# Performance work log

Hardware: AMD Instinct MI355X
Metric: run time of the kernel (lower is better)

Reference implementation:

```python
import jax, jax.numpy as jnp
import numpy as np

CLS_NUM, INPUT_DIM, BATCH = 1024, 512, 16384
TAU = 0.1       # gumbel-softmax temperature from F.gumbel_softmax(sim, tau=0.1)
EPS = 1e-12     # F.normalize eps


def _l2norm(x):
    # F.normalize(x, p=2, dim=1)
    n = jnp.sqrt(jnp.sum(x * x, axis=1, keepdims=True))
    return x / jnp.maximum(n, EPS)


def setup_inputs() -> dict:
    key = jax.random.key(0)
    k1, k2, k3 = jax.random.split(key, 3)
    # xavier_uniform bound for [cls_num, input_dim]
    bound = float(np.sqrt(6.0 / (CLS_NUM + INPUT_DIM)))
    return {
        "input": jax.random.normal(k1, (BATCH, INPUT_DIM), dtype=jnp.float32),
        "prototypes_para": jax.random.uniform(k2, (CLS_NUM, INPUT_DIM), dtype=jnp.float32, minval=-bound, maxval=bound),
        "gumbel_u": jax.random.uniform(k3, (BATCH, CLS_NUM), dtype=jnp.float32, minval=1e-6, maxval=1.0 - 1e-6),
    }


def reference(input, prototypes_para, gumbel_u):
    x = _l2norm(input)                 # [B, D]
    p = _l2norm(prototypes_para)       # [K, D]
    # Original: broadcast x and p to [B, K, D] (via multiply-by-ones) then cosine.
    # Since both are unit-norm, cosine similarity == dot product -> one matmul.
    # Input is .detach()'d in the original, so stop_gradient on x here.
    sim = jax.lax.stop_gradient(x) @ p.T                    # [B, K]
    # Gumbel-softmax (soft): softmax((logits + gumbel)/tau)
    g = -jnp.log(-jnp.log(gumbel_u))
    e = jax.nn.softmax((sim + g) / TAU, axis=-1)            # [B, K]
    pt = jnp.einsum('bk,kv->bv', e, p)                      # [B, D]
    sim_loss = jnp.mean(1.0 - jnp.einsum('bk,bk->b', e, sim))
    # Nested i!=j pairwise cosine loop == sum of P P^T minus its diagonal
    ppt = p @ p.T                                           # [K, K]
    div_loss = jnp.sum(ppt) - jnp.sum(jnp.diagonal(ppt))
    return pt, p, sim_loss, div_loss
```

## Files before the change

### kernel.cpp

```cpp
#include <hip/hip_runtime.h>
#include <math.h>

#define B  16384
#define K  1024
#define D  512
#define TAU_INV 10.0f
#define EPS 1e-12f

#define SM_C1 14.426950408889634f
#define SM_C2 5.287663729448977f

typedef unsigned short ushort_t;

#define LOG2F(x) __builtin_amdgcn_logf(x)
#define EXP2F(x) __builtin_amdgcn_exp2f(x)

#define OUT_PT   0
#define OUT_P    (B*D)
#define OUT_SIM  (B*D + K*D)
#define OUT_DIV  (B*D + K*D + 1)

#define WS_RED   1024
#define WS_SIM   32768
#define WS_PH    (WS_SIM + (B*K)/2)
#define WS_PTH   (WS_PH + (K*D)/2)
#define WS_DIAGP (WS_PTH + (K*D)/2)
#define WS_COLP  (WS_DIAGP + 256)


typedef _Float16 half8 __attribute__((ext_vector_type(8)));
typedef float f32x4 __attribute__((ext_vector_type(4)));

__device__ __forceinline__ float wave_reduce_sum(float v) {
    #pragma unroll
    for (int off = 32; off >= 1; off >>= 1) v += __shfl_down(v, off);
    return v;
}
__device__ __forceinline__ float wave_reduce_max(float v) {
    #pragma unroll
    for (int off = 32; off >= 1; off >>= 1) v = fmaxf(v, __shfl_down(v, off));
    return v;
}

__device__ __forceinline__ ushort_t f2h(float f) {
    _Float16 h = (_Float16)f;
    return __builtin_bit_cast(ushort_t, h);
}
__device__ __forceinline__ float h2f(ushort_t u) {
    return (float)__builtin_bit_cast(_Float16, u);
}

__device__ __forceinline__ void async16(const void* g, void* l) {
    __builtin_amdgcn_global_load_lds(
        (const __attribute__((address_space(1))) unsigned int*)g,
        (__attribute__((address_space(3))) unsigned int*)l, 16, 0, 0);
}

__global__ __launch_bounds__(256) void norm_p_kernel(const float* __restrict__ proto,
                                                     float* __restrict__ out,
                                                     float* __restrict__ ws,
                                                     ushort_t* __restrict__ Ph) {
    __shared__ float cs[4][512];
    __shared__ float red[4];
    int tid = threadIdx.x, wid = tid >> 6, lane = tid & 63;
    int row = blockIdx.x * 4 + wid;
    const float4* pr = (const float4*)(proto + (size_t)row * D);
    float4 a = pr[lane * 2], b = pr[lane * 2 + 1];
    float ss = a.x*a.x + a.y*a.y + a.z*a.z + a.w*a.w
             + b.x*b.x + b.y*b.y + b.z*b.z + b.w*b.w;
    ss = wave_reduce_sum(ss);
    ss = __shfl(ss, 0);
    float inv = 1.0f / fmaxf(sqrtf(ss), EPS);
    float4 na = make_float4(a.x*inv, a.y*inv, a.z*inv, a.w*inv);
    float4 nb = make_float4(b.x*inv, b.y*inv, b.z*inv, b.w*inv);
    float4* po = (float4*)(out + OUT_P + (size_t)row * D);
    po[lane * 2]     = na;
    po[lane * 2 + 1] = nb;
    ushort4* ph = (ushort4*)(Ph + (size_t)row * D);
    ph[lane * 2]     = make_ushort4(f2h(na.x), f2h(na.y), f2h(na.z), f2h(na.w));
    ph[lane * 2 + 1] = make_ushort4(f2h(nb.x), f2h(nb.y), f2h(nb.z), f2h(nb.w));
    *(float4*)(&cs[wid][lane * 8])     = na;
    *(float4*)(&cs[wid][lane * 8 + 4]) = nb;
    if (lane == 0) red[wid] = ss * inv * inv;
    __syncthreads();
    float c0 = cs[0][tid] + cs[1][tid] + cs[2][tid] + cs[3][tid];
    float c1 = cs[0][tid + 256] + cs[1][tid + 256] + cs[2][tid + 256] + cs[3][tid + 256];
    ws[WS_COLP + (size_t)blockIdx.x * 512 + tid]       = c0;
    ws[WS_COLP + (size_t)blockIdx.x * 512 + tid + 256] = c1;
    if (tid == 0) ws[WS_DIAGP + blockIdx.x] = red[0] + red[1] + red[2] + red[3];
}

__global__ __launch_bounds__(256) void ptcvt_kernel(const float* __restrict__ out,
                                                    ushort_t* __restrict__ PT) {
    __shared__ float tile[64][65];
    int k0 = blockIdx.x * 64, d0 = blockIdx.y * 64;
    int tid = threadIdx.x;
    const float* phat = out + OUT_P;
    #pragma unroll
    for (int i = tid; i < 64 * 64; i += 256) {
        int kk = i >> 6, dd = i & 63;
        tile[dd][kk] = phat[(size_t)(k0 + kk) * D + d0 + dd];
    }
    __syncthreads();
    #pragma unroll
    for (int i = tid; i < 64 * 64; i += 256) {
        int dd = i >> 6, kk = i & 63;
        PT[(size_t)(d0 + dd) * K + k0 + kk] = f2h(tile[dd][kk]);
    }
}

__global__ __launch_bounds__(256) void xcvt_kernel(const float* __restrict__ x,
                                                   ushort_t* __restrict__ Xh) {
    int wid = threadIdx.x >> 6, lane = threadIdx.x & 63;
    int row = blockIdx.x * 4 + wid;
    const float4* xr = (const float4*)(x + (size_t)row * D);
    float4 a = xr[lane * 2], b = xr[lane * 2 + 1];
    float ss = a.x*a.x + a.y*a.y + a.z*a.z + a.w*a.w
             + b.x*b.x + b.y*b.y + b.z*b.z + b.w*b.w;
    ss = wave_reduce_sum(ss);
    ss = __shfl(ss, 0);
    float inv = 1.0f / fmaxf(sqrtf(ss), EPS);
    ushort4 h0 = make_ushort4(f2h(a.x*inv), f2h(a.y*inv), f2h(a.z*inv), f2h(a.w*inv));
    ushort4 h1 = make_ushort4(f2h(b.x*inv), f2h(b.y*inv), f2h(b.z*inv), f2h(b.w*inv));
    ushort4* xo = (ushort4*)(Xh + (size_t)row * D);
    xo[lane * 2]     = h0;
    xo[lane * 2 + 1] = h1;
}

template<int LDA, int LDB, int LDC, int KK, bool F16C>
__global__ __launch_bounds__(256) void gemm_bt2(const ushort_t* __restrict__ A,
                                                const ushort_t* __restrict__ Bm,
                                                void* __restrict__ Cv) {
    __shared__ __align__(16) ushort_t As[2 * 128 * 32];
    __shared__ __align__(16) ushort_t Bs[2 * 128 * 32];
    int tid = threadIdx.x;
    int wid = tid >> 6, lane = tid & 63;
    int quad = lane >> 4, l16 = lane & 15;
    int wm = (wid & 1) * 64, wn = (wid >> 1) * 64;
    int bn0 = blockIdx.x * 128, bm0 = blockIdx.y * 128;
    int ldrow = lane >> 2;
    int lcol  = (lane & 3) * 8;

    f32x4 acc[4][4] = {};

    ushort_t* AsD[2][2] = {
        { As + (wid * 16) * 32,        As + (64 + wid * 16) * 32 },
        { As + 4096 + (wid * 16) * 32, As + 4096 + (64 + wid * 16) * 32 } };
    ushort_t* BsD[2][2] = {
        { Bs + (wid * 16) * 32,        Bs + (64 + wid * 16) * 32 },
        { Bs + 4096 + (wid * 16) * 32, Bs + 4096 + (64 + wid * 16) * 32 } };

    const ushort_t* Ab = A + (size_t)(bm0 + wid * 16 + ldrow) * LDA + lcol;
    const ushort_t* Bb = Bm + (size_t)(bn0 + wid * 16 + ldrow) * LDB + lcol;

    for (int kc = 0; kc < KK; kc += 64) {
        async16(Ab + kc,                       AsD[0][0]);
        async16(Ab + kc + (size_t)64 * LDA,    AsD[0][1]);
        async16(Ab + kc + 32,                  AsD[1][0]);
        async16(Ab + kc + 32 + (size_t)64*LDA, AsD[1][1]);
        async16(Bb + kc,                       BsD[0][0]);
        async16(Bb + kc + (size_t)64 * LDB,    BsD[0][1]);
        async16(Bb + kc + 32,                  BsD[1][0]);
        async16(Bb + kc + 32 + (size_t)64*LDB, BsD[1][1]);
        __syncthreads();
        #pragma unroll
        for (int p = 0; p < 2; ++p) {
            half8 af[4], bg[4];
            #pragma unroll
            for (int i = 0; i < 4; ++i)
                af[i] = *(const half8*)(As + p * 4096 + (wm + 16 * i + l16) * 32 + quad * 8);
            #pragma unroll
            for (int j = 0; j < 4; ++j)
                bg[j] = *(const half8*)(Bs + p * 4096 + (wn + 16 * j + l16) * 32 + quad * 8);
            #pragma unroll
            for (int i = 0; i < 4; ++i)
                #pragma unroll
                for (int j = 0; j < 4; ++j)
                    acc[i][j] = __builtin_amdgcn_mfma_f32_16x16x32_f16(af[i], bg[j], acc[i][j], 0, 0, 0);
        }
        __syncthreads();
    }
    #pragma unroll
    for (int i = 0; i < 4; ++i) {
        #pragma unroll
        for (int j = 0; j < 4; ++j) {
            #pragma unroll
            for (int r = 0; r < 4; ++r) {
                int row = bm0 + wm + 16 * i + quad * 4 + r;
                int col = bn0 + wn + 16 * j + l16;
                if (F16C)
                    ((ushort_t*)Cv)[(size_t)row * LDC + col] = f2h(acc[i][j][r]);
                else
                    ((float*)Cv)[(size_t)row * LDC + col] = acc[i][j][r];
            }
        }
    }
}

__global__ __launch_bounds__(256) void softmax_rows(const float* __restrict__ u,
                                                    float* __restrict__ ws) {
    ushort_t* simh = (ushort_t*)(ws + WS_SIM);
    int tid = threadIdx.x;
    int wid = tid >> 6, lane = tid & 63;
    int gw = blockIdx.x * 4 + wid;
    float dotacc = 0.0f;

    for (int r = 0; r < 4; ++r) {
        int row = gw + 4096 * r;
        ushort4* srow = (ushort4*)(simh + (size_t)row * K);
        const float4* urow = (const float4*)(u + (size_t)row * K);
        float4 s[4], z[4];
        #pragma unroll
        for (int j = 0; j < 4; ++j) {
            ushort4 sh = srow[lane + 64 * j];
            float4 uu = urow[lane + 64 * j];
            s[j] = make_float4(h2f(sh.x), h2f(sh.y), h2f(sh.z), h2f(sh.w));
            z[j].x = SM_C1 * s[j].x - 10.0f * LOG2F(-LOG2F(uu.x)) + SM_C2;
            z[j].y = SM_C1 * s[j].y - 10.0f * LOG2F(-LOG2F(uu.y)) + SM_C2;
            z[j].z = SM_C1 * s[j].z - 10.0f * LOG2F(-LOG2F(uu.z)) + SM_C2;
            z[j].w = SM_C1 * s[j].w - 10.0f * LOG2F(-LOG2F(uu.w)) + SM_C2;
        }
        float m = z[0].x;
        #pragma unroll
        for (int j = 0; j < 4; ++j)
            m = fmaxf(m, fmaxf(fmaxf(z[j].x, z[j].y), fmaxf(z[j].z, z[j].w)));
        m = wave_reduce_max(m);
        m = __shfl(m, 0);

        float4 e[4];
        float l = 0.0f;
        #pragma unroll
        for (int j = 0; j < 4; ++j) {
            e[j].x = EXP2F(z[j].x - m);
            e[j].y = EXP2F(z[j].y - m);
            e[j].z = EXP2F(z[j].z - m);
            e[j].w = EXP2F(z[j].w - m);
            l += e[j].x + e[j].y + e[j].z + e[j].w;
        }
        l = wave_reduce_sum(l);
        l = __shfl(l, 0);
        float inv = 1.0f / l;

        #pragma unroll
        for (int j = 0; j < 4; ++j) {
            float ex = e[j].x * inv, ey = e[j].y * inv,
                  ez = e[j].z * inv, ew = e[j].w * inv;
            srow[lane + 64 * j] = make_ushort4(f2h(ex), f2h(ey), f2h(ez), f2h(ew));
            dotacc += ex * s[j].x + ey * s[j].y + ez * s[j].z + ew * s[j].w;
        }
    }

    dotacc = wave_reduce_sum(dotacc);
    __shared__ float red[4];
    if (lane == 0) red[wid] = dotacc;
    __syncthreads();
    if (tid == 0) ws[WS_RED + blockIdx.x] = red[0] + red[1] + red[2] + red[3];
}

__global__ __launch_bounds__(1024) void finalize_kernel(float* __restrict__ out,
                                                        const float* __restrict__ ws) {
    __shared__ float cred[1024];
    __shared__ float rd[16], rs[16], rg[16];
    int tid = threadIdx.x, wid = tid >> 6, lane = tid & 63;
    int col = tid & 511, h = tid >> 9;
    float c = 0.0f;
    #pragma unroll 8
    for (int b2 = h * 128; b2 < h * 128 + 128; ++b2)
        c += ws[WS_COLP + (size_t)b2 * 512 + col];
    cred[tid] = c;
    float vdot = ws[WS_RED + tid];
    float diag = (tid < 256) ? ws[WS_DIAGP + tid] : 0.0f;
    __syncthreads();
    float vssq = 0.0f;
    if (tid < 512) {
        float cc = cred[tid] + cred[tid + 512];
        vssq = cc * cc;
    }
    vdot = wave_reduce_sum(vdot);
    vssq = wave_reduce_sum(vssq);
    diag = wave_reduce_sum(diag);
    if (lane == 0) { rd[wid] = vdot; rs[wid] = vssq; rg[wid] = diag; }
    __syncthreads();
    if (tid == 0) {
        float dot = 0.0f, ssq = 0.0f, dg = 0.0f;
        #pragma unroll
        for (int w = 0; w < 16; ++w) { dot += rd[w]; ssq += rs[w]; dg += rg[w]; }
        out[OUT_SIM] = 1.0f - dot * (1.0f / (float)B);
        out[OUT_DIV] = ssq - dg;
    }
}

extern "C" void kernel_launch(void* const* d_in, const int* in_sizes, int n_in,
                              void* d_out, int out_size, void* d_ws, size_t ws_size,
                              hipStream_t stream) {
    const float* input  = (const float*)d_in[0];
    const float* proto  = (const float*)d_in[1];
    const float* gumbel = (const float*)d_in[2];
    float* out = (float*)d_out;
    float* ws  = (float*)d_ws;

    ushort_t* Xh   = (ushort_t*)(out + OUT_PT);
    ushort_t* Ph   = (ushort_t*)(ws + WS_PH);
    ushort_t* PTh  = (ushort_t*)(ws + WS_PTH);
    ushort_t* simh = (ushort_t*)(ws + WS_SIM);

    norm_p_kernel<<<K / 4, 256, 0, stream>>>(proto, out, ws, Ph);
    {
        dim3 grid(K / 64, D / 64);
        ptcvt_kernel<<<grid, 256, 0, stream>>>(out, PTh);
    }
    xcvt_kernel<<<B / 4, 256, 0, stream>>>(input, Xh);
    {
        dim3 grid(K / 128, B / 128);
        gemm_bt2<512, 512, K, 512, true><<<grid, 256, 0, stream>>>(Xh, Ph, simh);
    }
    softmax_rows<<<1024, 256, 0, stream>>>(gumbel, ws);
    {
        dim3 grid(D / 128, B / 128);
        gemm_bt2<1024, 1024, D, 1024, false><<<grid, 256, 0, stream>>>(simh, PTh, out + OUT_PT);
    }
    finalize_kernel<<<1, 1024, 0, stream>>>(out, ws);
}
```

Measured before the change: 216.1 us.

## Replace 128x128 GEMM with 256-row double-buffered swizzled-LDS GEMM

Replaces the 128x128-tile GEMM with a templated 512-thread kernel using 256xBN tiles and 64-wide K slices. Shared-memory staging is now double-buffered and XOR-swizzled, with prefetch of the next slice interleaved into four compute phases and ordered by vmcnt waits and barriers. The larger tiles raise operand reuse per global load, the prefetch overlaps loads with MFMA work, and the swizzle avoids LDS bank conflicts. In exchange the kernel uses more registers and shared memory per block, and the grid shrinks, which may hurt occupancy or wave balance across CUs.

```diff
diff --git a/kernel.cpp b/kernel.cpp
--- a/kernel.cpp
+++ b/kernel.cpp
@@ -4,7 +4,6 @@
 #define B  16384
 #define K  1024
 #define D  512
-#define TAU_INV 10.0f
 #define EPS 1e-12f
 
 #define SM_C1 14.426950408889634f
@@ -127,63 +126,110 @@
     xo[lane * 2 + 1] = h1;
 }
 
-template<int LDA, int LDB, int LDC, int KK, bool F16C>
-__global__ __launch_bounds__(256) void gemm_bt2(const ushort_t* __restrict__ A,
-                                                const ushort_t* __restrict__ Bm,
-                                                void* __restrict__ Cv) {
-    __shared__ __align__(16) ushort_t As[2 * 128 * 32];
-    __shared__ __align__(16) ushort_t Bs[2 * 128 * 32];
+template<int BN, int LDA, int LDB, int LDC, int KK, bool F16C>
+__global__ __launch_bounds__(512, 2) void gemm256(const ushort_t* __restrict__ A,
+                                                  const ushort_t* __restrict__ Bm,
+                                                  void* __restrict__ Cv) {
+    constexpr int TJ  = BN / 64;
+    constexpr int TJH = TJ / 2;
+    constexpr int BCH = BN / 64;
+    constexpr int NT  = KK / 64;
+    __shared__ __align__(16) ushort_t As[2][256 * 64];
+    __shared__ __align__(16) ushort_t Bs[2][BN * 64];
+
     int tid = threadIdx.x;
     int wid = tid >> 6, lane = tid & 63;
     int quad = lane >> 4, l16 = lane & 15;
-    int wm = (wid & 1) * 64, wn = (wid >> 1) * 64;
-    int bn0 = blockIdx.x * 128, bm0 = blockIdx.y * 128;
-    int ldrow = lane >> 2;
-    int lcol  = (lane & 3) * 8;
-
-    f32x4 acc[4][4] = {};
-
-    ushort_t* AsD[2][2] = {
-        { As + (wid * 16) * 32,        As + (64 + wid * 16) * 32 },
-        { As + 4096 + (wid * 16) * 32, As + 4096 + (64 + wid * 16) * 32 } };
-    ushort_t* BsD[2][2] = {
-        { Bs + (wid * 16) * 32,        Bs + (64 + wid * 16) * 32 },
-        { Bs + 4096 + (wid * 16) * 32, Bs + 4096 + (64 + wid * 16) * 32 } };
-
-    const ushort_t* Ab = A + (size_t)(bm0 + wid * 16 + ldrow) * LDA + lcol;
-    const ushort_t* Bb = Bm + (size_t)(bn0 + wid * 16 + ldrow) * LDB + lcol;
-
-    for (int kc = 0; kc < KK; kc += 64) {
-        async16(Ab + kc,                       AsD[0][0]);
-        async16(Ab + kc + (size_t)64 * LDA,    AsD[0][1]);
-        async16(Ab + kc + 32,                  AsD[1][0]);
-        async16(Ab + kc + 32 + (size_t)64*LDA, AsD[1][1]);
-        async16(Bb + kc,                       BsD[0][0]);
-        async16(Bb + kc + (size_t)64 * LDB,    BsD[0][1]);
-        async16(Bb + kc + 32,                  BsD[1][0]);
-        async16(Bb + kc + 32 + (size_t)64*LDB, BsD[1][1]);
-        __syncthreads();
-        #pragma unroll
-        for (int p = 0; p < 2; ++p) {
-            half8 af[4], bg[4];
+    int wm = (wid & 1) * 128;
+    int wn = (wid >> 1) * (BN / 4);
+    int bn0 = blockIdx.x * BN, bm0 = blockIdx.y * 256;
+
+    f32x4 acc[8][TJ] = {};
+
+    auto stageA = [&](int buf, int kc, int q) {
+        int c = q * 512 + tid;
+        int row = c >> 3, sub = c & 7;
+        async16(A + (size_t)(bm0 + row) * LDA + kc + ((sub ^ (row & 7)) << 3),
+                &As[buf][(size_t)(q * 512 + wid * 64) * 8]);
+    };
+    auto stageB = [&](int buf, int kc, int q) {
+        int c = q * 512 + tid;
+        int row = c >> 3, sub = c & 7;
+        async16(Bm + (size_t)(bn0 + row) * LDB + kc + ((sub ^ (row & 7)) << 3),
+                &Bs[buf][(size_t)(q * 512 + wid * 64) * 8]);
+    };
+    auto rdA = [&](int buf, int r, int x) -> half8 {
+        return *(const half8*)(&As[buf][(size_t)r * 64 + ((x ^ (r & 7)) << 3)]);
+    };
+    auto rdB = [&](int buf, int r, int x) -> half8 {
+        return *(const half8*)(&Bs[buf][(size_t)r * 64 + ((x ^ (r & 7)) << 3)]);
+    };
+
+    #pragma unroll
+    for (int q = 0; q < 4; ++q) stageA(0, 0, q);
+    #pragma unroll
+    for (int q = 0; q < BCH; ++q) stageB(0, 0, q);
+    asm volatile("s_waitcnt vmcnt(0)" ::: "memory");
+    __builtin_amdgcn_s_barrier();
+
+    int cur = 0;
+    for (int t = 0; t < NT; ++t) {
+        int kc2 = (t + 1) * 64;
+        bool pf = (t + 1 < NT);
+        #pragma unroll
+        for (int p = 0; p < 4; ++p) {
+            if (p == 2) {
+                if (pf) asm volatile("s_waitcnt vmcnt(4)" ::: "memory");
+                else    asm volatile("s_waitcnt vmcnt(0)" ::: "memory");
+            }
+            if (pf) {
+                if (BN == 256) {
+                    if      (p == 0) { stageA(cur ^ 1, kc2, 0); stageA(cur ^ 1, kc2, 2); }
+                    else if (p == 1) { stageB(cur ^ 1, kc2, 0); stageB(cur ^ 1, kc2, 1); }
+                    else if (p == 2) { stageB(cur ^ 1, kc2, 2); stageB(cur ^ 1, kc2, 3); }
+                    else             { stageA(cur ^ 1, kc2, 1); stageA(cur ^ 1, kc2, 3); }
+                } else {
+                    if      (p == 0) { stageA(cur ^ 1, kc2, 0); stageA(cur ^ 1, kc2, 2); }
+                    else if (p == 1) { stageB(cur ^ 1, kc2, 0); stageB(cur ^ 1, kc2, 1); }
+                    else if (p == 2) { stageA(cur ^ 1, kc2, 1); }
+                    else             { stageA(cur ^ 1, kc2, 3); }
+                }
+            }
+            const int ih = p >> 1, jh = p & 1;
+            half8 af[4][2], bf[TJH][2];
             #pragma unroll
-            for (int i = 0; i < 4; ++i)
-                af[i] = *(const half8*)(As + p * 4096 + (wm + 16 * i + l16) * 32 + quad * 8);
+            for (int ii = 0; ii < 4; ++ii)
+                #pragma unroll
+                for (int ks = 0; ks < 2; ++ks)
+                    af[ii][ks] = rdA(cur, wm + (ih * 4 + ii) * 16 + l16, ks * 4 + quad);
             #pragma unroll
-            for (int j = 0; j < 4; ++j)
-                bg[j] = *(const half8*)(Bs + p * 4096 + (wn + 16 * j + l16) * 32 + quad * 8);
+            for (int jj = 0; jj < TJH; ++jj)
+                #pragma unroll
+                for (int ks = 0; ks < 2; ++ks)
+                    bf[jj][ks] = rdB(cur, wn + (jh * TJH + jj) * 16 + l16, ks * 4 + quad);
+            __builtin_amdgcn_s_setprio(1);
             #pragma unroll
-            for (int i = 0; i < 4; ++i)
+            for (int ii = 0; ii < 4; ++ii)
                 #pragma unroll
-                for (int j = 0; j < 4; ++j)
-                    acc[i][j] = __builtin_amdgcn_mfma_f32_16x16x32_f16(af[i], bg[j], acc[i][j], 0, 0, 0);
+                for (int jj = 0; jj < TJH; ++jj) {
+                    acc[ih*4+ii][jh*TJH+jj] = __builtin_amdgcn_mfma_f32_16x16x32_f16(
+                        af[ii][0], bf[jj][0], acc[ih*4+ii][jh*TJH+jj], 0, 0, 0);
+                    acc[ih*4+ii][jh*TJH+jj] = __builtin_amdgcn_mfma_f32_16x16x32_f16(
+                        af[ii][1], bf[jj][1], acc[ih*4+ii][jh*TJH+jj], 0, 0, 0);
+                }
+            __builtin_amdgcn_s_setprio(0);
+            if (p < 3) __builtin_amdgcn_s_barrier();
         }
-        __syncthreads();
-    }
-    #pragma unroll
-    for (int i = 0; i < 4; ++i) {
-        #pragma unroll
-        for (int j = 0; j < 4; ++j) {
+        if (pf) asm volatile("s_waitcnt vmcnt(2)" ::: "memory");
+        else    asm volatile("s_waitcnt vmcnt(0)" ::: "memory");
+        __builtin_amdgcn_s_barrier();
+        cur ^= 1;
+    }
+
+    #pragma unroll
+    for (int i = 0; i < 8; ++i)
+        #pragma unroll
+        for (int j = 0; j < TJ; ++j)
             #pragma unroll
             for (int r = 0; r < 4; ++r) {
                 int row = bm0 + wm + 16 * i + quad * 4 + r;
@@ -193,8 +239,6 @@
                 else
                     ((float*)Cv)[(size_t)row * LDC + col] = acc[i][j][r];
             }
-        }
-    }
 }
 
 __global__ __launch_bounds__(256) void softmax_rows(const float* __restrict__ u,
@@ -311,13 +355,13 @@
     }
     xcvt_kernel<<<B / 4, 256, 0, stream>>>(input, Xh);
     {
-        dim3 grid(K / 128, B / 128);
-        gemm_bt2<512, 512, K, 512, true><<<grid, 256, 0, stream>>>(Xh, Ph, simh);
+        dim3 grid(K / 256, B / 256);
+        gemm256<256, 512, 512, K, 512, true><<<grid, 512, 0, stream>>>(Xh, Ph, simh);
     }
     softmax_rows<<<1024, 256, 0, stream>>>(gumbel, ws);
     {
-        dim3 grid(D / 128, B / 128);
-        gemm_bt2<1024, 1024, D, 1024, false><<<grid, 256, 0, stream>>>(simh, PTh, out + OUT_PT);
+        dim3 grid(D / 128, B / 256);
+        gemm256<128, 1024, 1024, D, 1024, false><<<grid, 512, 0, stream>>>(simh, PTh, out + OUT_PT);
     }
     finalize_kernel<<<1, 1024, 0, stream>>>(out, ws);
 }
```

New measurement: 231.3 us. 1.07x slower.
